# Kernel tuning notes

Measured on AMD Instinct MI355X. Metric: run time of the kernel, lower is better.

## Reference

```python
import jax, jax.numpy as jnp
import numpy as np

H = 512
T = 512
B = 32

def _gru_layer(x_tm, mask_tm, W_ih, W_hh, b_ih, b_hh):
    # x_tm: [T, B, H] time-major input; mask_tm: [T, B, 1] bool (t < length)
    # Precompute input projections for all timesteps: [T, B, 3H]
    x_proj = jnp.einsum('tbi,gi->tbg', x_tm, W_ih) + b_ih

    def step(h, inp):
        xp, m = inp                      # xp: [B,3H], m: [B,1]
        hp = h @ W_hh.T + b_hh           # [B,3H]
        xr, xz, xn = jnp.split(xp, 3, axis=-1)
        hr, hz, hn = jnp.split(hp, 3, axis=-1)
        r = jax.nn.sigmoid(xr + hr)
        z = jax.nn.sigmoid(xz + hz)
        n = jnp.tanh(xn + r * hn)
        h_new = (1.0 - z) * n + z * h
        # packed-sequence semantics: hidden frozen past length, output zero past length
        h = jnp.where(m, h_new, h)
        y = jnp.where(m, h_new, jnp.zeros_like(h_new))
        return h, y

    h0 = jnp.zeros((x_tm.shape[1], W_hh.shape[1]), x_tm.dtype)
    _, ys = jax.lax.scan(step, h0, (x_proj, mask_tm))
    return ys  # [T, B, H]


def setup_inputs() -> dict:
    key = jax.random.key(0)
    ks = jax.random.split(key, 12)
    edu_hidden = jax.random.normal(ks[0], (B, T, H), dtype=jnp.float32)
    edu_lengths = jax.random.randint(ks[1], (B,), 1, T + 1)
    edu_lengths = edu_lengths.at[0].set(T)  # pad_packed output length == T
    s = 1.0 / np.sqrt(H)
    def U(k, shape):
        return jax.random.uniform(k, shape, jnp.float32, -s, s)
    return {
        'edu_hidden': edu_hidden,
        'edu_lengths': edu_lengths,
        'W_ih_0': U(ks[2], (3 * H, H)), 'W_hh_0': U(ks[3], (3 * H, H)),
        'b_ih_0': U(ks[4], (3 * H,)),   'b_hh_0': U(ks[5], (3 * H,)),
        'W_ih_1': U(ks[6], (3 * H, H)), 'W_hh_1': U(ks[7], (3 * H, H)),
        'b_ih_1': U(ks[8], (3 * H,)),   'b_hh_1': U(ks[9], (3 * H,)),
    }


def reference(edu_hidden, edu_lengths, W_ih_0, W_hh_0, b_ih_0, b_hh_0,
              W_ih_1, W_hh_1, b_ih_1, b_hh_1):
    # mask[t, b] = t < edu_lengths[b]
    t_idx = jnp.arange(T)
    mask_tm = (t_idx[:, None] < edu_lengths[None, :])[:, :, None]  # [T, B, 1]
    x = jnp.transpose(edu_hidden, (1, 0, 2))  # time-major [T, B, H]
    x = _gru_layer(x, mask_tm, W_ih_0, W_hh_0, b_ih_0, b_hh_0)
    x = _gru_layer(x, mask_tm, W_ih_1, W_hh_1, b_ih_1, b_hh_1)
    return jnp.transpose(x, (1, 0, 2))  # [B, T, H], zeros past each length
```

## Files before the change

kernel.cpp:

```cpp
#include <hip/hip_runtime.h>
#include <cstdint>
#include <cstddef>

#define Hdim 512
#define Tdim 512
#define Bdim 32
#define NWG  256
#define SCAN_THREADS 384

typedef float        f32x4 __attribute__((ext_vector_type(4)));
typedef unsigned int u32x4 __attribute__((ext_vector_type(4)));
typedef unsigned int u32x2 __attribute__((ext_vector_type(2)));

__device__ __forceinline__ float sigmoidf_(float v) {
    return 1.f / (1.f + __expf(-v));
}
__device__ __forceinline__ float tanhf_(float a) {
    float ax = fabsf(a);
    float e  = __expf(-2.f * ax);
    float t  = (1.f - e) / (1.f + e);
    return copysignf(t, a);
}

__global__ void __launch_bounds__(SCAN_THREADS, 1)
gru_scan(const float* __restrict__ xp,
         const float* __restrict__ Whh,
         const float* __restrict__ bhh,
         const int*   __restrict__ lens,
         float*       __restrict__ y,
         u32x2*       hb2,
         int t0, int Tc)
{
    __shared__ float  hlf[4 * Hdim];
    __shared__ float4 part4[8 * 49];

    const int tid = threadIdx.x;
    const int wg  = blockIdx.x;
    const int u   = wg & 31;
    const int bg  = wg >> 5;
    const int j0  = u << 4;
    const int b0  = bg << 2;
    const int rw  = tid >> 5;
    const int kq  = tid & 31;

    float4 w[4][4];
#pragma unroll
    for (int i = 0; i < 4; ++i) {
        int r = rw + 12 * i;
        const float* p = Whh + ((size_t)(((r >> 4) << 9) + j0 + (r & 15)) << 9) + (kq << 2);
#pragma unroll
        for (int c = 0; c < 4; ++c) w[i][c] = *(const float4*)(p + (c << 7));
    }

    const bool isGate = tid < 64;
    const int gjl = tid & 15;
    const int gb  = (tid >> 4) & 3;
    const int jg  = j0 + gjl;
    int   glen = 0;
    float bh_r = 0.f, bh_z = 0.f, bh_n = 0.f;
    const float* xpb = nullptr;
    if (isGate) {
        glen = lens[b0 + gb];
        bh_r = bhh[jg];
        bh_z = bhh[512 + jg];
        bh_n = bhh[1024 + jg];
        xpb = xp + (size_t)(b0 + gb) * Tc * 1536;
    }

    const bool isPoll = tid < 256;
    const int  pb  = tid >> 6;
    const int  pL  = (tid & 63) << 1;
    float* lds_w0 = &hlf[(pb << 9) + (pL << 2)];
    float* lds_w1 = lds_w0 + 4;

    float xr = 0.f, xz = 0.f, xn = 0.f;
    if (isGate) {
        xr = xpb[jg];
        xz = xpb[512 + jg];
        xn = xpb[1024 + jg];
    }

    int budget = 1 << 20;

    for (int t = t0; t < t0 + Tc; ++t) {
        const unsigned tg = (unsigned)t;

        if (isPoll) {
            const u32x2* src = hb2 + ((size_t)(t & 1) << 14) + (bg << 11) + (tid << 3);
            u32x4 q0, q1, q2, q3;
            for (;;) {
                asm volatile(
                    "global_load_dwordx4 %0, %4, off sc0 sc1\n\t"
                    "global_load_dwordx4 %1, %4, off offset:16 sc0 sc1\n\t"
                    "global_load_dwordx4 %2, %4, off offset:32 sc0 sc1\n\t"
                    "global_load_dwordx4 %3, %4, off offset:48 sc0 sc1\n\t"
                    "s_waitcnt vmcnt(0)"
                    : "=&v"(q0), "=&v"(q1), "=&v"(q2), "=&v"(q3)
                    : "v"(src) : "memory");
                bool ok = (q0[1] == tg) & (q0[3] == tg) & (q1[1] == tg) & (q1[3] == tg) &
                          (q2[1] == tg) & (q2[3] == tg) & (q3[1] == tg) & (q3[3] == tg);
                if (__all(ok)) break;
                if (--budget < 0) break;
            }
            f32x4 h0 = { __uint_as_float(q0[0]), __uint_as_float(q0[2]),
                         __uint_as_float(q1[0]), __uint_as_float(q1[2]) };
            f32x4 h1 = { __uint_as_float(q2[0]), __uint_as_float(q2[2]),
                         __uint_as_float(q3[0]), __uint_as_float(q3[2]) };
            *(f32x4*)lds_w0 = h0;
            *(f32x4*)lds_w1 = h1;
        }
        float xrn = 0.f, xzn = 0.f, xnn = 0.f;
        if (isGate) {
            int tf = (t + 1 < t0 + Tc) ? (t + 1 - t0) : (t - t0);
            const float* xq = xpb + (size_t)tf * 1536;
            xrn = xq[jg];
            xzn = xq[512 + jg];
            xnn = xq[1024 + jg];
        }
        __syncthreads();

        float acc[4][4];
#pragma unroll
        for (int i = 0; i < 4; ++i)
#pragma unroll
            for (int b = 0; b < 4; ++b) acc[i][b] = 0.f;
#pragma unroll
        for (int b = 0; b < 4; ++b) {
            const float4* hb4 = (const float4*)&hlf[b << 9];
            float4 h0 = hb4[kq];
            float4 h1 = hb4[kq + 32];
            float4 h2 = hb4[kq + 64];
            float4 h3 = hb4[kq + 96];
#pragma unroll
            for (int i = 0; i < 4; ++i) {
                float a = acc[i][b];
                a = fmaf(w[i][0].x, h0.x, a); a = fmaf(w[i][0].y, h0.y, a);
                a = fmaf(w[i][0].z, h0.z, a); a = fmaf(w[i][0].w, h0.w, a);
                a = fmaf(w[i][1].x, h1.x, a); a = fmaf(w[i][1].y, h1.y, a);
                a = fmaf(w[i][1].z, h1.z, a); a = fmaf(w[i][1].w, h1.w, a);
                a = fmaf(w[i][2].x, h2.x, a); a = fmaf(w[i][2].y, h2.y, a);
                a = fmaf(w[i][2].z, h2.z, a); a = fmaf(w[i][2].w, h2.w, a);
                a = fmaf(w[i][3].x, h3.x, a); a = fmaf(w[i][3].y, h3.y, a);
                a = fmaf(w[i][3].z, h3.z, a); a = fmaf(w[i][3].w, h3.w, a);
                acc[i][b] = a;
            }
        }
#pragma unroll
        for (int mm = 1; mm <= 2; mm <<= 1)
#pragma unroll
            for (int i = 0; i < 4; ++i)
#pragma unroll
                for (int b = 0; b < 4; ++b)
                    acc[i][b] += __shfl_xor(acc[i][b], mm);
        if ((kq & 3) == 0) {
            int mp = kq >> 2;
#pragma unroll
            for (int i = 0; i < 4; ++i)
                part4[mp * 49 + rw + 12 * i] =
                    make_float4(acc[i][0], acc[i][1], acc[i][2], acc[i][3]);
        }
        __syncthreads();

        if (isGate) {
            const float* pf = (const float*)part4;
            float s0 = 0.f, s1 = 0.f, s2 = 0.f;
#pragma unroll
            for (int m = 0; m < 8; ++m) {
                int base = ((m * 49 + gjl) << 2) + gb;
                s0 += pf[base];
                s1 += pf[base + 64];
                s2 += pf[base + 128];
            }
            float hold = hlf[(gb << 9) + jg];
            float rr = sigmoidf_(xr + s0 + bh_r);
            float zz = sigmoidf_(xz + s1 + bh_z);
            float nn = tanhf_(xn + rr * (s2 + bh_n));
            float hnew = (1.f - zz) * nn + zz * hold;
            bool msk = t < glen;
            float hnext = msk ? hnew : hold;
            y[((size_t)(b0 + gb) * Tdim + t) * Hdim + jg] = msk ? hnew : 0.f;
            u32x2 pv;
            pv[0] = __float_as_uint(hnext);
            pv[1] = (unsigned)(t + 1);
            u32x2* dst = hb2 + ((size_t)((t + 1) & 1) << 14) + (bg << 11) + (gb << 9) + jg;
            asm volatile("global_store_dwordx2 %0, %1, off sc0 sc1"
                         :: "v"(dst), "v"(pv) : "memory");
            xr = xrn; xz = xzn; xn = xnn;
        }
        __syncthreads();
    }
}

#define FMA4(c, a, b) { (c).x = fmaf((a), (b).x, (c).x); (c).y = fmaf((a), (b).y, (c).y); \
                        (c).z = fmaf((a), (b).z, (c).z); (c).w = fmaf((a), (b).w, (c).w); }

__global__ void __launch_bounds__(256)
gemm_xproj(const float* __restrict__ A,
           const float* __restrict__ W,
           const float* __restrict__ bias,
           float* __restrict__ C,
           int tcLog, int t0)
{
    __shared__ float As[16][132];
    __shared__ float Bs[16][132];
    const int tid = threadIdx.x;
    const int n0  = blockIdx.x << 7;
    const int m0  = blockIdx.y << 7;
    const int tx  = tid & 15;
    const int ty  = tid >> 4;

    const int mrow = tid >> 2;
    const int kcol = (tid & 3) << 2;
    const int Tcm1 = (1 << tcLog) - 1;

    int mg0 = m0 + mrow;
    int mg1 = m0 + 64 + mrow;
    size_t srow0 = (size_t)(mg0 >> tcLog) * Tdim + t0 + (mg0 & Tcm1);
    size_t srow1 = (size_t)(mg1 >> tcLog) * Tdim + t0 + (mg1 & Tcm1);
    const float* Ap0 = A + srow0 * Hdim + kcol;
    const float* Ap1 = A + srow1 * Hdim + kcol;
    const float* Wp0 = W + (size_t)(n0 + mrow) * Hdim + kcol;
    const float* Wp1 = W + (size_t)(n0 + 64 + mrow) * Hdim + kcol;

    float4 c00[4], c01[4], c10[4], c11[4];
#pragma unroll
    for (int i = 0; i < 4; ++i) {
        c00[i] = {0.f,0.f,0.f,0.f}; c01[i] = {0.f,0.f,0.f,0.f};
        c10[i] = {0.f,0.f,0.f,0.f}; c11[i] = {0.f,0.f,0.f,0.f};
    }

    float4 a0 = *(const float4*)(Ap0);
    float4 a1 = *(const float4*)(Ap1);
    float4 b0 = *(const float4*)(Wp0);
    float4 b1 = *(const float4*)(Wp1);

    for (int kt = 0; kt < 512; kt += 16) {
        __syncthreads();
        As[kcol+0][mrow] = a0.x; As[kcol+1][mrow] = a0.y;
        As[kcol+2][mrow] = a0.z; As[kcol+3][mrow] = a0.w;
        As[kcol+0][mrow+64] = a1.x; As[kcol+1][mrow+64] = a1.y;
        As[kcol+2][mrow+64] = a1.z; As[kcol+3][mrow+64] = a1.w;
        Bs[kcol+0][mrow] = b0.x; Bs[kcol+1][mrow] = b0.y;
        Bs[kcol+2][mrow] = b0.z; Bs[kcol+3][mrow] = b0.w;
        Bs[kcol+0][mrow+64] = b1.x; Bs[kcol+1][mrow+64] = b1.y;
        Bs[kcol+2][mrow+64] = b1.z; Bs[kcol+3][mrow+64] = b1.w;
        __syncthreads();
        if (kt + 16 < 512) {
            a0 = *(const float4*)(Ap0 + kt + 16);
            a1 = *(const float4*)(Ap1 + kt + 16);
            b0 = *(const float4*)(Wp0 + kt + 16);
            b1 = *(const float4*)(Wp1 + kt + 16);
        }
#pragma unroll
        for (int kk = 0; kk < 16; ++kk) {
            float4 aA = *(const float4*)&As[kk][ty * 4];
            float4 aB = *(const float4*)&As[kk][64 + ty * 4];
            float4 bA = *(const float4*)&Bs[kk][tx * 4];
            float4 bB = *(const float4*)&Bs[kk][64 + tx * 4];
            FMA4(c00[0], aA.x, bA); FMA4(c01[0], aA.x, bB);
            FMA4(c00[1], aA.y, bA); FMA4(c01[1], aA.y, bB);
            FMA4(c00[2], aA.z, bA); FMA4(c01[2], aA.z, bB);
            FMA4(c00[3], aA.w, bA); FMA4(c01[3], aA.w, bB);
            FMA4(c10[0], aB.x, bA); FMA4(c11[0], aB.x, bB);
            FMA4(c10[1], aB.y, bA); FMA4(c11[1], aB.y, bB);
            FMA4(c10[2], aB.z, bA); FMA4(c11[2], aB.z, bB);
            FMA4(c10[3], aB.w, bA); FMA4(c11[3], aB.w, bB);
        }
    }

    float4 biasA = *(const float4*)(bias + n0 + tx * 4);
    float4 biasB = *(const float4*)(bias + n0 + 64 + tx * 4);
#pragma unroll
    for (int i = 0; i < 4; ++i) {
        size_t row0 = (size_t)m0 + ty * 4 + i;
        size_t row1 = row0 + 64;
        float4 v;
        v.x = c00[i].x + biasA.x; v.y = c00[i].y + biasA.y;
        v.z = c00[i].z + biasA.z; v.w = c00[i].w + biasA.w;
        *(float4*)(C + row0 * 1536 + n0 + tx * 4) = v;
        v.x = c01[i].x + biasB.x; v.y = c01[i].y + biasB.y;
        v.z = c01[i].z + biasB.z; v.w = c01[i].w + biasB.w;
        *(float4*)(C + row0 * 1536 + n0 + 64 + tx * 4) = v;
        v.x = c10[i].x + biasA.x; v.y = c10[i].y + biasA.y;
        v.z = c10[i].z + biasA.z; v.w = c10[i].w + biasA.w;
        *(float4*)(C + row1 * 1536 + n0 + tx * 4) = v;
        v.x = c11[i].x + biasB.x; v.y = c11[i].y + biasB.y;
        v.z = c11[i].z + biasB.z; v.w = c11[i].w + biasB.w;
        *(float4*)(C + row1 * 1536 + n0 + 64 + tx * 4) = v;
    }
}

extern "C" void kernel_launch(void* const* d_in, const int* in_sizes, int n_in,
                              void* d_out, int out_size, void* d_ws, size_t ws_size,
                              hipStream_t stream) {
    (void)in_sizes; (void)n_in; (void)out_size;
    const float* x    = (const float*)d_in[0];
    const int*   lens = (const int*)d_in[1];
    const float* Wih0 = (const float*)d_in[2];
    const float* Whh0 = (const float*)d_in[3];
    const float* bih0 = (const float*)d_in[4];
    const float* bhh0 = (const float*)d_in[5];
    const float* Wih1 = (const float*)d_in[6];
    const float* Whh1 = (const float*)d_in[7];
    const float* bih1 = (const float*)d_in[8];
    const float* bhh1 = (const float*)d_in[9];
    float* out = (float*)d_out;

    const size_t hb2_bytes  = (size_t)2 * 8 * 2048 * 8;
    const size_t ctrl_bytes = 2 * hb2_bytes;
    int Tc = 512;
    while (Tc > 4 && (size_t)Bdim * Tc * 1536 * 4 + ctrl_bytes > ws_size) Tc >>= 1;
    int tcLog = 31 - __builtin_clz((unsigned)Tc);
    size_t xp_bytes = (size_t)Bdim * Tc * 1536 * 4;

    float* xp = (float*)d_ws;
    char*  ctrl = (char*)d_ws + xp_bytes;
    u32x2* hb2_0 = (u32x2*)ctrl;
    u32x2* hb2_1 = (u32x2*)(ctrl + hb2_bytes);

    (void)hipMemsetAsync(ctrl, 0, ctrl_bytes, stream);

    const int nChunks = Tdim / Tc;
    for (int layer = 0; layer < 2; ++layer) {
        const float* src  = layer ? (const float*)out : x;
        const float* Wih  = layer ? Wih1 : Wih0;
        const float* bih  = layer ? bih1 : bih0;
        const float* Whh  = layer ? Whh1 : Whh0;
        const float* bhhp = layer ? bhh1 : bhh0;
        u32x2* hb2 = layer ? hb2_1 : hb2_0;

        for (int c = 0; c < nChunks; ++c) {
            int t0 = c * Tc;
            dim3 gg(12, (Bdim * Tc) >> 7);
            gemm_xproj<<<gg, dim3(256), 0, stream>>>(src, Wih, bih, xp, tcLog, t0);

            const float* a_xp  = xp;
            const float* a_whh = Whh;
            const float* a_bhh = bhhp;
            const int*   a_ln  = lens;
            float*       a_y   = out;
            u32x2*       a_hb  = hb2;
            int a_t0 = t0;
            int a_tc = Tc;
            void* args[] = { &a_xp, &a_whh, &a_bhh, &a_ln, &a_y, &a_hb, &a_t0, &a_tc };
            (void)hipLaunchCooperativeKernel((const void*)gru_scan, dim3(NWG),
                                             dim3(SCAN_THREADS), args, 0, stream);
        }
    }
}
```

Before: 3.717 ms.

## Fuse both GRU layers into one wavefront-pipelined scan with fp16 register weights

Adds a single cooperative kernel that runs layer 0 at step i and layer 1 at step i-1 in the same iteration. It keeps W_hh0, W_hh1 and W_ih1 resident in registers as packed fp16 and uses fdot2 for the mat-vecs. This removes the second scan launch, the layer-1 input-projection GEMM and one full set of serial cross-workgroup syncs, halving the dependent step count. The cost is three mat-vecs and a triple-sized flag poll per step, plus fp16 rounding of weights and hidden state, which may hurt accuracy.

```diff
diff --git a/kernel.cpp b/kernel.cpp
--- a/kernel.cpp
+++ b/kernel.cpp
@@ -11,6 +11,8 @@
 typedef float        f32x4 __attribute__((ext_vector_type(4)));
 typedef unsigned int u32x4 __attribute__((ext_vector_type(4)));
 typedef unsigned int u32x2 __attribute__((ext_vector_type(2)));
+typedef _Float16     h16x2 __attribute__((ext_vector_type(2)));
+typedef _Float16     h16x8 __attribute__((ext_vector_type(8)));
 
 __device__ __forceinline__ float sigmoidf_(float v) {
     return 1.f / (1.f + __expf(-v));
@@ -21,15 +23,249 @@
     float t  = (1.f - e) / (1.f + e);
     return copysignf(t, a);
 }
+__device__ __forceinline__ h16x2 pk2(float a, float b) {
+    h16x2 r; r[0] = (_Float16)a; r[1] = (_Float16)b; return r;
+}
 
 __global__ void __launch_bounds__(SCAN_THREADS, 1)
-gru_scan(const float* __restrict__ xp,
-         const float* __restrict__ Whh,
-         const float* __restrict__ bhh,
-         const int*   __restrict__ lens,
-         float*       __restrict__ y,
-         u32x2*       hb2,
-         int t0, int Tc)
+gru_fused(const float* __restrict__ xp,
+          const float* __restrict__ Whh0,
+          const float* __restrict__ bhh0,
+          const float* __restrict__ Whh1,
+          const float* __restrict__ bhh1,
+          const float* __restrict__ Wih1,
+          const float* __restrict__ bih1,
+          const int*   __restrict__ lens,
+          float*       __restrict__ y,
+          u32x2*       hb)
+{
+    __shared__ h16x2  hl[3][4][256];
+    __shared__ float4 part4[24 * 49];
+
+    const int tid = threadIdx.x;
+    const int wg  = blockIdx.x;
+    const int u   = wg & 31, bg = wg >> 5;
+    const int j0  = u << 4,  b0 = bg << 2;
+    const int rw  = tid >> 5;
+    const int kq  = tid & 31;
+
+    h16x2 w0[4][8], w1[4][8], wx[4][8];
+#pragma unroll
+    for (int i = 0; i < 4; ++i) {
+        int r = rw + 12 * i;
+        size_t grow = (size_t)(((r >> 4) << 9) + j0 + (r & 15)) << 9;
+        const float* pa = Whh0 + grow + (kq << 3);
+        const float* pb = Whh1 + grow + (kq << 3);
+        const float* pc = Wih1 + grow + (kq << 3);
+#pragma unroll
+        for (int c = 0; c < 2; ++c) {
+            float4 q0 = *(const float4*)(pa + (c << 8));
+            float4 q1 = *(const float4*)(pa + (c << 8) + 4);
+            w0[i][4*c+0] = pk2(q0.x, q0.y); w0[i][4*c+1] = pk2(q0.z, q0.w);
+            w0[i][4*c+2] = pk2(q1.x, q1.y); w0[i][4*c+3] = pk2(q1.z, q1.w);
+            q0 = *(const float4*)(pb + (c << 8));
+            q1 = *(const float4*)(pb + (c << 8) + 4);
+            w1[i][4*c+0] = pk2(q0.x, q0.y); w1[i][4*c+1] = pk2(q0.z, q0.w);
+            w1[i][4*c+2] = pk2(q1.x, q1.y); w1[i][4*c+3] = pk2(q1.z, q1.w);
+            q0 = *(const float4*)(pc + (c << 8));
+            q1 = *(const float4*)(pc + (c << 8) + 4);
+            wx[i][4*c+0] = pk2(q0.x, q0.y); wx[i][4*c+1] = pk2(q0.z, q0.w);
+            wx[i][4*c+2] = pk2(q1.x, q1.y); wx[i][4*c+3] = pk2(q1.z, q1.w);
+        }
+    }
+
+    const bool isGate = tid < 64;
+    const int gjl = tid & 15;
+    const int gb  = (tid >> 4) & 3;
+    const int jg  = j0 + gjl;
+    int   glen = 0;
+    float bh0r=0,bh0z=0,bh0n=0, bh1r=0,bh1z=0,bh1n=0, bxr=0,bxz=0,bxn=0;
+    float h0reg = 0.f, h1reg = 0.f;
+    const float* xpb = nullptr;
+    if (isGate) {
+        glen = lens[b0 + gb];
+        bh0r = bhh0[jg]; bh0z = bhh0[512 + jg]; bh0n = bhh0[1024 + jg];
+        bh1r = bhh1[jg]; bh1z = bhh1[512 + jg]; bh1n = bhh1[1024 + jg];
+        bxr  = bih1[jg]; bxz  = bih1[512 + jg]; bxn  = bih1[1024 + jg];
+        xpb = xp + (size_t)(b0 + gb) * Tdim * 1536;
+    }
+
+    const bool isPoll = tid < 256;
+    const int  pb = tid >> 6;
+    const int  u8 = tid & 63;
+
+    float xr = 0.f, xz = 0.f, xn = 0.f;
+    if (isGate) { xr = xpb[jg]; xz = xpb[512 + jg]; xn = xpb[1024 + jg]; }
+
+    int budget = 1 << 20;
+
+    for (int i = 0; i <= Tdim; ++i) {
+        const unsigned tg = (unsigned)i;
+
+        if (isPoll) {
+            const u32x2* sA = hb + (size_t)(i & 1) * 49152
+                               + (size_t)((bg << 2) + pb) * 512 + (u8 << 3);
+            const u32x2* sB = sA + 16384;
+            const u32x2* sC = sA + 32768;
+            u32x4 qa0,qa1,qa2,qa3, qb0,qb1,qb2,qb3, qc0,qc1,qc2,qc3;
+            for (;;) {
+                asm volatile(
+                    "global_load_dwordx4 %0, %12, off sc0 sc1\n\t"
+                    "global_load_dwordx4 %1, %12, off offset:16 sc0 sc1\n\t"
+                    "global_load_dwordx4 %2, %12, off offset:32 sc0 sc1\n\t"
+                    "global_load_dwordx4 %3, %12, off offset:48 sc0 sc1\n\t"
+                    "global_load_dwordx4 %4, %13, off sc0 sc1\n\t"
+                    "global_load_dwordx4 %5, %13, off offset:16 sc0 sc1\n\t"
+                    "global_load_dwordx4 %6, %13, off offset:32 sc0 sc1\n\t"
+                    "global_load_dwordx4 %7, %13, off offset:48 sc0 sc1\n\t"
+                    "global_load_dwordx4 %8, %14, off sc0 sc1\n\t"
+                    "global_load_dwordx4 %9, %14, off offset:16 sc0 sc1\n\t"
+                    "global_load_dwordx4 %10, %14, off offset:32 sc0 sc1\n\t"
+                    "global_load_dwordx4 %11, %14, off offset:48 sc0 sc1\n\t"
+                    "s_waitcnt vmcnt(0)"
+                    : "=&v"(qa0), "=&v"(qa1), "=&v"(qa2), "=&v"(qa3),
+                      "=&v"(qb0), "=&v"(qb1), "=&v"(qb2), "=&v"(qb3),
+                      "=&v"(qc0), "=&v"(qc1), "=&v"(qc2), "=&v"(qc3)
+                    : "v"(sA), "v"(sB), "v"(sC) : "memory");
+                bool ok = (qa0[1]==tg)&(qa0[3]==tg)&(qa1[1]==tg)&(qa1[3]==tg)
+                        & (qa2[1]==tg)&(qa2[3]==tg)&(qa3[1]==tg)&(qa3[3]==tg)
+                        & (qb0[1]==tg)&(qb0[3]==tg)&(qb1[1]==tg)&(qb1[3]==tg)
+                        & (qb2[1]==tg)&(qb2[3]==tg)&(qb3[1]==tg)&(qb3[3]==tg)
+                        & (qc0[1]==tg)&(qc0[3]==tg)&(qc1[1]==tg)&(qc1[3]==tg)
+                        & (qc2[1]==tg)&(qc2[3]==tg)&(qc3[1]==tg)&(qc3[3]==tg);
+                if (__all(ok)) break;
+                if (--budget < 0) break;
+            }
+            h16x8 v;
+            v[0]=(_Float16)__uint_as_float(qa0[0]); v[1]=(_Float16)__uint_as_float(qa0[2]);
+            v[2]=(_Float16)__uint_as_float(qa1[0]); v[3]=(_Float16)__uint_as_float(qa1[2]);
+            v[4]=(_Float16)__uint_as_float(qa2[0]); v[5]=(_Float16)__uint_as_float(qa2[2]);
+            v[6]=(_Float16)__uint_as_float(qa3[0]); v[7]=(_Float16)__uint_as_float(qa3[2]);
+            ((h16x8*)&hl[0][pb][0])[u8] = v;
+            v[0]=(_Float16)__uint_as_float(qb0[0]); v[1]=(_Float16)__uint_as_float(qb0[2]);
+            v[2]=(_Float16)__uint_as_float(qb1[0]); v[3]=(_Float16)__uint_as_float(qb1[2]);
+            v[4]=(_Float16)__uint_as_float(qb2[0]); v[5]=(_Float16)__uint_as_float(qb2[2]);
+            v[6]=(_Float16)__uint_as_float(qb3[0]); v[7]=(_Float16)__uint_as_float(qb3[2]);
+            ((h16x8*)&hl[1][pb][0])[u8] = v;
+            v[0]=(_Float16)__uint_as_float(qc0[0]); v[1]=(_Float16)__uint_as_float(qc0[2]);
+            v[2]=(_Float16)__uint_as_float(qc1[0]); v[3]=(_Float16)__uint_as_float(qc1[2]);
+            v[4]=(_Float16)__uint_as_float(qc2[0]); v[5]=(_Float16)__uint_as_float(qc2[2]);
+            v[6]=(_Float16)__uint_as_float(qc3[0]); v[7]=(_Float16)__uint_as_float(qc3[2]);
+            ((h16x8*)&hl[2][pb][0])[u8] = v;
+        }
+        float xrn = 0.f, xzn = 0.f, xnn = 0.f;
+        if (isGate && i < Tdim) {
+            int tf = (i + 1 < Tdim) ? i + 1 : i;
+            const float* xq = xpb + (size_t)tf * 1536;
+            xrn = xq[jg]; xzn = xq[512 + jg]; xnn = xq[1024 + jg];
+        }
+        __syncthreads();
+
+#define MATVEC(W, MIDX) do {                                                  \
+        float acc[4][4] = {};                                                 \
+        _Pragma("unroll")                                                     \
+        for (int b = 0; b < 4; ++b) {                                         \
+            const h16x8* hp = (const h16x8*)&hl[MIDX][b][0];                  \
+            h16x8 v0 = hp[kq], v1 = hp[kq + 32];                              \
+            h16x2 e0={v0[0],v0[1]}, e1={v0[2],v0[3]},                         \
+                  e2={v0[4],v0[5]}, e3={v0[6],v0[7]};                         \
+            h16x2 f0={v1[0],v1[1]}, f1={v1[2],v1[3]},                         \
+                  f2={v1[4],v1[5]}, f3={v1[6],v1[7]};                         \
+            _Pragma("unroll")                                                 \
+            for (int ii = 0; ii < 4; ++ii) {                                  \
+                float a = acc[ii][b];                                         \
+                a = __builtin_amdgcn_fdot2(W[ii][0], e0, a, false);           \
+                a = __builtin_amdgcn_fdot2(W[ii][1], e1, a, false);           \
+                a = __builtin_amdgcn_fdot2(W[ii][2], e2, a, false);           \
+                a = __builtin_amdgcn_fdot2(W[ii][3], e3, a, false);           \
+                a = __builtin_amdgcn_fdot2(W[ii][4], f0, a, false);           \
+                a = __builtin_amdgcn_fdot2(W[ii][5], f1, a, false);           \
+                a = __builtin_amdgcn_fdot2(W[ii][6], f2, a, false);           \
+                a = __builtin_amdgcn_fdot2(W[ii][7], f3, a, false);           \
+                acc[ii][b] = a;                                               \
+            }                                                                 \
+        }                                                                     \
+        _Pragma("unroll")                                                     \
+        for (int mm = 1; mm <= 2; mm <<= 1)                                   \
+            _Pragma("unroll")                                                 \
+            for (int ii = 0; ii < 4; ++ii)                                    \
+                _Pragma("unroll")                                             \
+                for (int b = 0; b < 4; ++b)                                   \
+                    acc[ii][b] += __shfl_xor(acc[ii][b], mm);                 \
+        if ((kq & 3) == 0) {                                                  \
+            int mp = kq >> 2;                                                 \
+            _Pragma("unroll")                                                 \
+            for (int ii = 0; ii < 4; ++ii)                                    \
+                part4[((MIDX) * 8 + mp) * 49 + rw + 12 * ii] =                \
+                    make_float4(acc[ii][0], acc[ii][1], acc[ii][2], acc[ii][3]); \
+        }                                                                     \
+    } while (0)
+
+        MATVEC(w0, 0);
+        MATVEC(w1, 1);
+        MATVEC(wx, 2);
+#undef MATVEC
+        __syncthreads();
+
+        if (isGate) {
+            const float* pf = (const float*)part4;
+            u32x2* d = hb + (size_t)((i + 1) & 1) * 49152
+                        + (size_t)((bg << 2) + gb) * 512 + jg;
+            if (i < Tdim) {
+                float s0 = 0.f, s1 = 0.f, s2 = 0.f;
+#pragma unroll
+                for (int mp = 0; mp < 8; ++mp) {
+                    int base = ((mp * 49 + gjl) << 2) + gb;
+                    s0 += pf[base];
+                    s1 += pf[base + 64];
+                    s2 += pf[base + 128];
+                }
+                float rr = sigmoidf_(xr + s0 + bh0r);
+                float zz = sigmoidf_(xz + s1 + bh0z);
+                float nn = tanhf_(xn + rr * (s2 + bh0n));
+                float h0new = (1.f - zz) * nn + zz * h0reg;
+                bool msk = i < glen;
+                h0reg = msk ? h0new : h0reg;
+                float y0v = msk ? h0new : 0.f;
+                u32x2 p0; p0[0] = __float_as_uint(h0reg); p0[1] = (unsigned)(i + 1);
+                u32x2 p2; p2[0] = __float_as_uint(y0v);   p2[1] = (unsigned)(i + 1);
+                asm volatile("global_store_dwordx2 %0, %1, off sc0 sc1"
+                             :: "v"(d), "v"(p0) : "memory");
+                asm volatile("global_store_dwordx2 %0, %1, off sc0 sc1"
+                             :: "v"(d + 32768), "v"(p2) : "memory");
+                xr = xrn; xz = xzn; xn = xnn;
+            }
+            if (i > 0) {
+                int s = i - 1;
+                float t0_=0.f, t1_=0.f, t2_=0.f, x0_=0.f, x1_=0.f, x2_=0.f;
+#pragma unroll
+                for (int mp = 0; mp < 8; ++mp) {
+                    int b1 = (((8 + mp) * 49 + gjl) << 2) + gb;
+                    int b2 = (((16 + mp) * 49 + gjl) << 2) + gb;
+                    t0_ += pf[b1]; t1_ += pf[b1 + 64]; t2_ += pf[b1 + 128];
+                    x0_ += pf[b2]; x1_ += pf[b2 + 64]; x2_ += pf[b2 + 128];
+                }
+                float rr = sigmoidf_(x0_ + bxr + t0_ + bh1r);
+                float zz = sigmoidf_(x1_ + bxz + t1_ + bh1z);
+                float nn = tanhf_(x2_ + bxn + rr * (t2_ + bh1n));
+                float h1new = (1.f - zz) * nn + zz * h1reg;
+                bool msk = s < glen;
+                h1reg = msk ? h1new : h1reg;
+                y[((size_t)(b0 + gb) * Tdim + s) * Hdim + jg] = msk ? h1new : 0.f;
+            }
+            if (i < Tdim) {
+                u32x2 p1; p1[0] = __float_as_uint(h1reg); p1[1] = (unsigned)(i + 1);
+                asm volatile("global_store_dwordx2 %0, %1, off sc0 sc1"
+                             :: "v"(d + 16384), "v"(p1) : "memory");
+            }
+        }
+    }
+}
+
+__global__ void __launch_bounds__(SCAN_THREADS, 1)
+gru_scan(const float* __restrict__ xp, const float* __restrict__ Whh,
+         const float* __restrict__ bhh, const int* __restrict__ lens,
+         float* __restrict__ y, u32x2* hb2, int t0, int Tc)
 {
     __shared__ float  hlf[4 * Hdim];
     __shared__ float4 part4[8 * 49];
@@ -61,9 +297,7 @@
     const float* xpb = nullptr;
     if (isGate) {
         glen = lens[b0 + gb];
-        bh_r = bhh[jg];
-        bh_z = bhh[512 + jg];
-        bh_n = bhh[1024 + jg];
+        bh_r = bhh[jg]; bh_z = bhh[512 + jg]; bh_n = bhh[1024 + jg];
         xpb = xp + (size_t)(b0 + gb) * Tc * 1536;
     }
 
@@ -74,17 +308,12 @@
     float* lds_w1 = lds_w0 + 4;
 
     float xr = 0.f, xz = 0.f, xn = 0.f;
-    if (isGate) {
-        xr = xpb[jg];
-        xz = xpb[512 + jg];
-        xn = xpb[1024 + jg];
-    }
+    if (isGate) { xr = xpb[jg]; xz = xpb[512 + jg]; xn = xpb[1024 + jg]; }
 
     int budget = 1 << 20;
 
     for (int t = t0; t < t0 + Tc; ++t) {
         const unsigned tg = (unsigned)t;
-
         if (isPoll) {
             const u32x2* src = hb2 + ((size_t)(t & 1) << 14) + (bg << 11) + (tid << 3);
             u32x4 q0, q1, q2, q3;
@@ -113,9 +342,7 @@
         if (isGate) {
             int tf = (t + 1 < t0 + Tc) ? (t + 1 - t0) : (t - t0);
             const float* xq = xpb + (size_t)tf * 1536;
-            xrn = xq[jg];
-            xzn = xq[512 + jg];
-            xnn = xq[1024 + jg];
+            xrn = xq[jg]; xzn = xq[512 + jg]; xnn = xq[1024 + jg];
         }
         __syncthreads();
 
@@ -306,45 +533,58 @@
     const float* bhh1 = (const float*)d_in[9];
     float* out = (float*)d_out;
 
-    const size_t hb2_bytes  = (size_t)2 * 8 * 2048 * 8;
-    const size_t ctrl_bytes = 2 * hb2_bytes;
+    const size_t hb_bytes = (size_t)2 * 3 * 8 * 2048 * 8;
     int Tc = 512;
-    while (Tc > 4 && (size_t)Bdim * Tc * 1536 * 4 + ctrl_bytes > ws_size) Tc >>= 1;
+    while (Tc > 4 && (size_t)Bdim * Tc * 1536 * 4 + hb_bytes > ws_size) Tc >>= 1;
     int tcLog = 31 - __builtin_clz((unsigned)Tc);
     size_t xp_bytes = (size_t)Bdim * Tc * 1536 * 4;
 
     float* xp = (float*)d_ws;
-    char*  ctrl = (char*)d_ws + xp_bytes;
-    u32x2* hb2_0 = (u32x2*)ctrl;
-    u32x2* hb2_1 = (u32x2*)(ctrl + hb2_bytes);
-
-    (void)hipMemsetAsync(ctrl, 0, ctrl_bytes, stream);
-
-    const int nChunks = Tdim / Tc;
-    for (int layer = 0; layer < 2; ++layer) {
-        const float* src  = layer ? (const float*)out : x;
-        const float* Wih  = layer ? Wih1 : Wih0;
-        const float* bih  = layer ? bih1 : bih0;
-        const float* Whh  = layer ? Whh1 : Whh0;
-        const float* bhhp = layer ? bhh1 : bhh0;
-        u32x2* hb2 = layer ? hb2_1 : hb2_0;
-
-        for (int c = 0; c < nChunks; ++c) {
-            int t0 = c * Tc;
-            dim3 gg(12, (Bdim * Tc) >> 7);
-            gemm_xproj<<<gg, dim3(256), 0, stream>>>(src, Wih, bih, xp, tcLog, t0);
-
-            const float* a_xp  = xp;
-            const float* a_whh = Whh;
-            const float* a_bhh = bhhp;
-            const int*   a_ln  = lens;
-            float*       a_y   = out;
-            u32x2*       a_hb  = hb2;
-            int a_t0 = t0;
-            int a_tc = Tc;
-            void* args[] = { &a_xp, &a_whh, &a_bhh, &a_ln, &a_y, &a_hb, &a_t0, &a_tc };
-            (void)hipLaunchCooperativeKernel((const void*)gru_scan, dim3(NWG),
-                                             dim3(SCAN_THREADS), args, 0, stream);
-        }
-    }
-}
+    u32x2* hb = (u32x2*)((char*)d_ws + xp_bytes);
+
+    (void)hipMemsetAsync(hb, 0, hb_bytes, stream);
+
+    if (Tc == 512) {
+        dim3 gg(12, (Bdim * 512) >> 7);
+        gemm_xproj<<<gg, dim3(256), 0, stream>>>(x, Wih0, bih0, xp, 9, 0);
+        const float* a_xp = xp;
+        const float* a_w0 = Whh0;  const float* a_b0 = bhh0;
+        const float* a_w1 = Whh1;  const float* a_b1 = bhh1;
+        const float* a_wx = Wih1;  const float* a_bx = bih1;
+        const int*   a_ln = lens;
+        float*       a_y  = out;
+        u32x2*       a_hb = hb;
+        void* args[] = { &a_xp, &a_w0, &a_b0, &a_w1, &a_b1, &a_wx, &a_bx,
+                         &a_ln, &a_y, &a_hb };
+        (void)hipLaunchCooperativeKernel((const void*)gru_fused, dim3(NWG),
+                                         dim3(SCAN_THREADS), args, 0, stream);
+    } else {
+        u32x2* hb2_0 = hb;
+        u32x2* hb2_1 = hb + 32768;
+        const int nChunks = Tdim / Tc;
+        for (int layer = 0; layer < 2; ++layer) {
+            const float* src  = layer ? (const float*)out : x;
+            const float* Wih  = layer ? Wih1 : Wih0;
+            const float* bih  = layer ? bih1 : bih0;
+            const float* Whh  = layer ? Whh1 : Whh0;
+            const float* bhhp = layer ? bhh1 : bhh0;
+            u32x2* hb2 = layer ? hb2_1 : hb2_0;
+            for (int c = 0; c < nChunks; ++c) {
+                int t0 = c * Tc;
+                dim3 gg(12, (Bdim * Tc) >> 7);
+                gemm_xproj<<<gg, dim3(256), 0, stream>>>(src, Wih, bih, xp, tcLog, t0);
+                const float* a_xp  = xp;
+                const float* a_whh = Whh;
+                const float* a_bhh = bhhp;
+                const int*   a_ln  = lens;
+                float*       a_y   = out;
+                u32x2*       a_hb  = hb2;
+                int a_t0 = t0;
+                int a_tc = Tc;
+                void* args[] = { &a_xp, &a_whh, &a_bhh, &a_ln, &a_y, &a_hb, &a_t0, &a_tc };
+                (void)hipLaunchCooperativeKernel((const void*)gru_scan, dim3(NWG),
+                                                 dim3(SCAN_THREADS), args, 0, stream);
+            }
+        }
+    }
+}
```

After: 6.287 ms. 69.2% more time.
